# Optimization experiments

Hardware: AMD Instinct MI355X
Metric: run time of the kernel (lower is better)

The kernel has to match this reference:

```python
import jax, jax.numpy as jnp
import numpy as np

EPS = 1e-9
LAM_SEL, LAM_ID, LAM_RATE, LAM_KL, LAM_ENT, LAM_SMOOTH = 1.0, 10.0, 5.0, 0.1, 0.05, 0.5


def setup_inputs() -> dict:
    T, BS, V, K, RIDS = 48, 256, 4096, 32, 1024
    key = jax.random.key(0)
    ks = jax.random.split(key, 10)
    selector_logits = jax.random.normal(ks[0], (BS, 2, K), dtype=jnp.float32)
    selector_probs = jax.nn.softmax(jax.random.normal(ks[1], (BS, 2, K)), axis=-1)
    sel_idx = jax.random.randint(ks[2], (BS, 2), 0, K)
    selector_onehot = jax.nn.one_hot(sel_idx, K, dtype=jnp.float32)
    out_ids = jax.nn.softmax(jax.random.normal(ks[3], (T, BS, V)), axis=-1)
    out_rates = jax.random.uniform(ks[4], (T, BS, 1), dtype=jnp.float32)
    lab_idx = jax.random.randint(ks[5], (T + 2, BS), 0, V)
    trg_labels = jax.nn.one_hot(lab_idx, V, dtype=jnp.float32)
    trg_rates = jax.random.uniform(ks[6], (T + 2, BS, 1), dtype=jnp.float32)
    trg_lengths = jax.random.randint(ks[7], (BS,), 4, T + 2).astype(jnp.int32)
    candi_ids = jax.random.randint(ks[8], (BS, 2, K), 0, RIDS).astype(jnp.int32)
    routes = jax.random.randint(ks[9], (BS, V), 0, RIDS).astype(jnp.int32)
    return {
        'selector_logits': selector_logits, 'selector_probs': selector_probs,
        'selector_onehot': selector_onehot, 'out_ids': out_ids, 'out_rates': out_rates,
        'trg_labels': trg_labels, 'trg_rates': trg_rates, 'trg_lengths': trg_lengths,
        'candi_ids': candi_ids, 'routes': routes,
    }


def _align(lab, T_pred):
    T_lab = lab.shape[0]
    if T_lab >= T_pred + 2:
        return lab[1:-1]
    elif T_lab == T_pred:
        return lab
    else:
        pad = T_pred - T_lab
        return jnp.concatenate([lab, jnp.repeat(lab[-1:], pad, axis=0)], axis=0)


def _loss(selector_logits, selector_probs, selector_onehot, out_ids, out_rates,
          trg_labels, trg_rates, trg_lengths, candi_ids, routes):
    bs, _, K = selector_probs.shape
    # --- selector NLL (use_bce_logits=False path) ---
    sel_mask = (selector_onehot.sum(-1) > 0.5).astype(jnp.float32)      # [bs,2]
    sel_p_true = jnp.maximum((selector_probs * selector_onehot).sum(-1), EPS)
    loss_sel = (-jnp.log(sel_p_true) * sel_mask).sum() / jnp.maximum(sel_mask.sum(), 1.0)

    # --- id NLL over aligned target labels ---
    T_pred = out_ids.shape[0]
    tla = _align(trg_labels, T_pred)                                    # [T,bs,V]
    tra = _align(trg_rates, T_pred)                                     # [T,bs,1]
    step_mask = (tla.sum(-1) > 0.5).astype(jnp.float32)                 # [T,bs]
    p_true = jnp.maximum((out_ids * tla).sum(-1), EPS)
    loss_id = (-jnp.log(p_true) * step_mask).sum() * LAM_ID / jnp.maximum(step_mask.sum(), 1.0)

    # --- rate L1 ---
    denom_rate = jnp.maximum(1, (trg_lengths - 2).sum()).astype(jnp.float32)
    loss_rate = jnp.abs(out_rates - tra).sum() * LAM_RATE / denom_rate

    # --- KL over per-batch candidate unions (vectorized dedup via first-occurrence) ---
    U2 = 2 * K
    ids = candi_ids.reshape(bs, U2)                                     # [bs,2K]
    probs_flat = selector_probs.reshape(bs, U2)                         # [bs,2K]
    eq = ids[:, :, None] == ids[:, None, :]                             # [bs,2K,2K]
    rep = jnp.argmax(eq, axis=-1)                                       # first occurrence idx
    slots = jnp.arange(U2)
    valid = (rep == slots[None, :]).astype(jnp.float32)                 # [bs,2K] union slots
    Ucnt = valid.sum(-1)                                                # [bs]
    # Pm: scatter-add selector probs onto union slots (duplicates summed)
    rep_oh = (rep[:, :, None] == slots[None, None, :]).astype(jnp.float32)  # [bs,2K,2K]
    Pm = jnp.einsum('biu,bi->bu', rep_oh, probs_flat)                   # [bs,2K]
    Pm = Pm / jnp.maximum(Pm.sum(-1, keepdims=True), EPS)
    # Pb: project route mass onto union ids
    dist_r = out_ids.sum(0)                                             # [bs,V]
    match = (routes[:, :, None] == ids[:, None, :]).astype(jnp.float32)  # [bs,V,2K]
    agg = jnp.einsum('bvu,bv->bu', match, dist_r) * valid               # [bs,2K]
    s = agg.sum(-1, keepdims=True)                                      # [bs,1]
    uniform = valid / jnp.maximum(Ucnt, 1.0)[:, None]
    Pb = jnp.where(s > 0, agg / jnp.maximum(s, EPS), uniform)
    Pb_c = jnp.maximum(Pb, EPS)
    kl_b = (Pb_c * (jnp.log(Pb_c) - jnp.log(jnp.maximum(Pm, EPS))) * valid).sum(-1)
    loss_kl = LAM_KL * (kl_b.sum() / max(1, bs))

    # --- entropy of selector probs ---
    p = jnp.maximum(selector_probs, EPS)                                # [bs,2,K]
    ent_b = 0.5 * (-(p * jnp.log(p)).sum(-1)).sum(-1)                   # [bs]
    loss_entropy = LAM_ENT * (ent_b.sum() / max(1, bs))

    # --- rate smoothness ---
    r = out_rates[..., 0]                                               # [T,bs]
    dr = jnp.abs(r[1:] - r[:-1])                                        # [T-1,bs]
    eff = jnp.maximum(trg_lengths - 3, 0)                               # [bs]
    smask = (jnp.arange(T_pred - 1)[:, None] < eff[None, :]).astype(jnp.float32)
    loss_smooth = LAM_SMOOTH * (dr * smask).sum()

    return LAM_SEL * loss_sel + loss_id + loss_rate + loss_kl + loss_entropy + loss_smooth


def reference(selector_logits, selector_probs, selector_onehot, out_ids, out_rates,
              trg_labels, trg_rates, trg_lengths, candi_ids, routes):
    return _loss(selector_logits, selector_probs, selector_onehot, out_ids, out_rates,
                 trg_labels, trg_rates, trg_lengths, candi_ids, routes)
```

## Files before the change

kernel.cpp:

```cpp
#include <hip/hip_runtime.h>
#include <math.h>

#define EPSF 1e-9f

typedef float v4f __attribute__((ext_vector_type(4)));


__global__ __launch_bounds__(256) void e2e3_prep(
    const float* __restrict__ selector_probs,
    const int*   __restrict__ candi_ids,
    const int*   __restrict__ routes,
    float* __restrict__ pmlog_g,
    float* __restrict__ valid_g,
    signed char* __restrict__ slot_map)
{
    const int b   = blockIdx.x;
    const int tid = threadIdx.x;

    __shared__ int   ids_s[64];
    __shared__ int   table[1024];
    __shared__ int   rep_s[64];

    for (int i = tid; i < 1024; i += 256) table[i] = 64;
    if (tid < 64) ids_s[tid] = candi_ids[b * 64 + tid];
    __syncthreads();
    if (tid < 64) atomicMin(&table[ids_s[tid]], tid);
    __syncthreads();
    if (tid < 64) {
        const int r = table[ids_s[tid]];
        rep_s[tid] = r;
        valid_g[b * 64 + tid] = (r == tid) ? 1.f : 0.f;
    }
    __syncthreads();
    if (tid < 64) {
        float pm = 0.f;
        for (int i = 0; i < 64; ++i)
            if (rep_s[i] == tid) pm += selector_probs[b * 64 + i];
        float tot = pm;
        #pragma unroll
        for (int off = 32; off >= 1; off >>= 1) tot += __shfl_xor(tot, off, 64);
        pm = pm / fmaxf(tot, EPSF);
        pmlog_g[b * 64 + tid] = logf(fmaxf(pm, EPSF));
    }

    const int4* rp = reinterpret_cast<const int4*>(routes + (size_t)b * 4096 + tid * 16);
    signed char smv[16];
    #pragma unroll
    for (int j = 0; j < 4; ++j) {
        const int4 rv = rp[j];
        const int t0 = table[rv.x], t1 = table[rv.y], t2 = table[rv.z], t3 = table[rv.w];
        smv[j * 4 + 0] = (signed char)(t0 < 64 ? t0 : -1);
        smv[j * 4 + 1] = (signed char)(t1 < 64 ? t1 : -1);
        smv[j * 4 + 2] = (signed char)(t2 < 64 ? t2 : -1);
        smv[j * 4 + 3] = (signed char)(t3 < 64 ? t3 : -1);
    }
    *reinterpret_cast<int4*>(slot_map + (size_t)b * 4096 + tid * 16) =
        *reinterpret_cast<const int4*>(smv);
}

__global__ __launch_bounds__(512) void e2e3_stream(
    const float* __restrict__ out_ids,
    const float* __restrict__ trg_labels,
    const signed char* __restrict__ slot_map,
    float* __restrict__ agg_g,
    float* __restrict__ acc)
{
    const int bid  = blockIdx.x;
    const int b    = bid & 255;
    const int g    = bid >> 8;
    const int tid  = threadIdx.x;
    const int wave = tid >> 6;
    const int lane = tid & 63;
    const int v0   = tid << 3;
    const int t0   = g * 12;

    __shared__ float agg_s[64];
    __shared__ float red[2][8];
    if (tid < 64) agg_s[tid] = 0.f;
    __syncthreads();

    const size_t tstride = (size_t)256 * 4096;
    const float* outp = out_ids    + (size_t)t0 * tstride       + (size_t)b * 4096 + v0;
    const float* labp = trg_labels + (size_t)(t0 + 1) * tstride + (size_t)b * 4096 + v0;

    v4f d0 = (v4f)(0.f);
    v4f d1 = (v4f)(0.f);
    float idnum = 0.f, idcnt = 0.f;

    v4f o0 = *reinterpret_cast<const v4f*>(outp);
    v4f o1 = *reinterpret_cast<const v4f*>(outp + 4);
    v4f l0 = __builtin_nontemporal_load(reinterpret_cast<const v4f*>(labp));
    v4f l1 = __builtin_nontemporal_load(reinterpret_cast<const v4f*>(labp + 4));

    for (int t = 0; t < 12; ++t) {
        v4f no0 = o0, no1 = o1, nl0 = l0, nl1 = l1;
        if (t < 11) {
            const size_t off = (size_t)(t + 1) * tstride;
            no0 = *reinterpret_cast<const v4f*>(outp + off);
            no1 = *reinterpret_cast<const v4f*>(outp + off + 4);
            nl0 = __builtin_nontemporal_load(reinterpret_cast<const v4f*>(labp + off));
            nl1 = __builtin_nontemporal_load(reinterpret_cast<const v4f*>(labp + off + 4));
        }
        d0 += o0;
        d1 += o1;
        if (l0.x > 0.5f) { idnum -= logf(fmaxf(o0.x, EPSF)); idcnt += 1.f; }
        if (l0.y > 0.5f) { idnum -= logf(fmaxf(o0.y, EPSF)); idcnt += 1.f; }
        if (l0.z > 0.5f) { idnum -= logf(fmaxf(o0.z, EPSF)); idcnt += 1.f; }
        if (l0.w > 0.5f) { idnum -= logf(fmaxf(o0.w, EPSF)); idcnt += 1.f; }
        if (l1.x > 0.5f) { idnum -= logf(fmaxf(o1.x, EPSF)); idcnt += 1.f; }
        if (l1.y > 0.5f) { idnum -= logf(fmaxf(o1.y, EPSF)); idcnt += 1.f; }
        if (l1.z > 0.5f) { idnum -= logf(fmaxf(o1.z, EPSF)); idcnt += 1.f; }
        if (l1.w > 0.5f) { idnum -= logf(fmaxf(o1.w, EPSF)); idcnt += 1.f; }
        o0 = no0; o1 = no1; l0 = nl0; l1 = nl1;
    }

    {
        const uint2 sv = *reinterpret_cast<const uint2*>(slot_map + (size_t)b * 4096 + v0);
        const unsigned int w0 = sv.x, w1 = sv.y;
        const float dv[8] = {d0.x, d0.y, d0.z, d0.w, d1.x, d1.y, d1.z, d1.w};
        #pragma unroll
        for (int j = 0; j < 4; ++j) {
            const int u0 = (int)(signed char)((w0 >> (8 * j)) & 0xFF);
            if (u0 >= 0) atomicAdd(&agg_s[u0], dv[j]);
            const int u1 = (int)(signed char)((w1 >> (8 * j)) & 0xFF);
            if (u1 >= 0) atomicAdd(&agg_s[u1], dv[4 + j]);
        }
    }

    #pragma unroll
    for (int off = 32; off >= 1; off >>= 1) {
        idnum += __shfl_down(idnum, off, 64);
        idcnt += __shfl_down(idcnt, off, 64);
    }
    if (lane == 0) { red[0][wave] = idnum; red[1][wave] = idcnt; }
    __syncthreads();
    if (tid == 0) {
        float a = 0.f, c = 0.f;
        #pragma unroll
        for (int w = 0; w < 8; ++w) { a += red[0][w]; c += red[1][w]; }
        atomicAdd(&acc[0], a);
        atomicAdd(&acc[1], c);
    }
    if (tid < 64) atomicAdd(&agg_g[b * 64 + tid], agg_s[tid]);
}

__global__ __launch_bounds__(64) void e2e3_kl2(
    const float* __restrict__ agg_g,
    const float* __restrict__ pmlog_g,
    const float* __restrict__ valid_g,
    float* __restrict__ acc)
{
    const int b = blockIdx.x;
    const int u = threadIdx.x;

    const float va = valid_g[b * 64 + u];
    const float a  = (va > 0.5f) ? agg_g[b * 64 + u] : 0.f;
    float s = a, uc = va;
    #pragma unroll
    for (int off = 32; off >= 1; off >>= 1) {
        s  += __shfl_xor(s,  off, 64);
        uc += __shfl_xor(uc, off, 64);
    }
    const float pb = (s > 0.f) ? (a / fmaxf(s, EPSF)) : (va / fmaxf(uc, 1.f));
    float term = 0.f;
    if (va > 0.5f) {
        const float pbc = fmaxf(pb, EPSF);
        term = pbc * (logf(pbc) - pmlog_g[b * 64 + u]);
    }
    #pragma unroll
    for (int off = 32; off >= 1; off >>= 1) term += __shfl_down(term, off, 64);
    if (u == 0) atomicAdd(&acc[2], term);
}

__global__ __launch_bounds__(256) void e2e3_small(
    const float* __restrict__ selector_probs,
    const float* __restrict__ selector_onehot,
    const float* __restrict__ out_rates,
    const float* __restrict__ trg_rates,
    const int*   __restrict__ trg_lengths,
    const float* __restrict__ acc,
    float* __restrict__ out)
{
    const int tid  = threadIdx.x;
    const int wave = tid >> 6;
    const int lane = tid & 63;

    float v_selnum = 0.f, v_selcnt = 0.f, v_ent = 0.f;
    float v_rate = 0.f, v_den = 0.f, v_smooth = 0.f;

    for (int g = tid; g < 512; g += 256) {
        const float* pp = selector_probs  + g * 32;
        const float* oo = selector_onehot + g * 32;
        float p = 0.f, m = 0.f;
        #pragma unroll
        for (int k = 0; k < 32; ++k) { p += pp[k] * oo[k]; m += oo[k]; }
        if (m > 0.5f) { v_selnum += -logf(fmaxf(p, EPSF)); v_selcnt += 1.f; }
    }
    for (int i = tid; i < 256 * 64; i += 256) {
        const float p = fmaxf(selector_probs[i], EPSF);
        v_ent += -p * logf(p);
    }
    for (int i = tid; i < 48 * 256; i += 256)
        v_rate += fabsf(out_rates[i] - trg_rates[i + 256]);
    for (int b2 = tid; b2 < 256; b2 += 256)
        v_den += (float)(trg_lengths[b2] - 2);
    for (int i = tid; i < 47 * 256; i += 256) {
        const int b2 = i & 255;
        const int t  = i >> 8;
        int eff = trg_lengths[b2] - 3; if (eff < 0) eff = 0;
        if (t < eff) v_smooth += fabsf(out_rates[i + 256] - out_rates[i]);
    }

    __shared__ float red[6][4];
    float vals[6] = {v_selnum, v_selcnt, v_ent, v_rate, v_den, v_smooth};
    #pragma unroll
    for (int k = 0; k < 6; ++k) {
        float v = vals[k];
        #pragma unroll
        for (int off = 32; off >= 1; off >>= 1) v += __shfl_down(v, off, 64);
        if (lane == 0) red[k][wave] = v;
    }
    __syncthreads();
    if (tid == 0) {
        float s[6];
        #pragma unroll
        for (int k = 0; k < 6; ++k) s[k] = red[k][0] + red[k][1] + red[k][2] + red[k][3];
        const float loss =
              s[0] / fmaxf(s[1], 1.f)
            + 10.f * acc[0] / fmaxf(acc[1], 1.f)
            + 5.f  * s[3]   / fmaxf(s[4], 1.f)
            + 0.1f * acc[2] * (1.f / 256.f)
            + 0.05f * 0.5f * s[2] * (1.f / 256.f)
            + 0.5f * s[5];
        out[0] = loss;
    }
}

extern "C" void kernel_launch(void* const* d_in, const int* in_sizes, int n_in,
                              void* d_out, int out_size, void* d_ws, size_t ws_size,
                              hipStream_t stream) {
    const float* selector_probs  = (const float*)d_in[1];
    const float* selector_onehot = (const float*)d_in[2];
    const float* out_ids         = (const float*)d_in[3];
    const float* out_rates       = (const float*)d_in[4];
    const float* trg_labels      = (const float*)d_in[5];
    const float* trg_rates       = (const float*)d_in[6];
    const int*   trg_lengths     = (const int*)d_in[7];
    const int*   candi_ids       = (const int*)d_in[8];
    const int*   routes          = (const int*)d_in[9];

    char* ws = (char*)d_ws;
    float*       acc      = (float*)ws;
    float*       agg_g    = (float*)(ws + 256);
    float*       pmlog_g  = (float*)(ws + 256 + 65536);
    float*       valid_g  = (float*)(ws + 256 + 131072);
    signed char* slot_map = (signed char*)(ws + 256 + 196608);

    (void)hipMemsetAsync(ws, 0, 256 + 65536, stream);

    e2e3_prep<<<256, 256, 0, stream>>>(selector_probs, candi_ids, routes,
                                       pmlog_g, valid_g, slot_map);
    e2e3_stream<<<1024, 512, 0, stream>>>(out_ids, trg_labels, slot_map,
                                          agg_g, acc);
    e2e3_kl2<<<256, 64, 0, stream>>>(agg_g, pmlog_g, valid_g, acc);
    e2e3_small<<<1, 256, 0, stream>>>(selector_probs, selector_onehot,
                                      out_rates, trg_rates, trg_lengths,
                                      acc, (float*)d_out);
}
```

Baseline: 122.1 us.

## Split label scan into hot-index kernel and gather id NLL in streaming pass

A new kernel scans each one-hot label row once and records the index of its hot entry. The out_ids streaming kernel then no longer reads labels; it does one gather and one log per timestep for the NLL instead of a compare and possible log for every element. It also now prefetches two timesteps ahead. Total label and out_ids traffic stays the same but is split across two launches. The scan assumes at most one hot entry per row, and the extra launch adds a dependency.

```diff
diff --git a/kernel.cpp b/kernel.cpp
--- a/kernel.cpp
+++ b/kernel.cpp
@@ -58,10 +58,42 @@
         *reinterpret_cast<const int4*>(smv);
 }
 
-__global__ __launch_bounds__(512) void e2e3_stream(
+__global__ __launch_bounds__(256) void e2e3_hot(
+    const float* __restrict__ trg_labels,
+    int* __restrict__ hot_idx)
+{
+    const int wave = threadIdx.x >> 6;
+    const int lane = threadIdx.x & 63;
+    const int row  = blockIdx.x * 4 + wave;
+    const int t    = row >> 8;
+    const int b    = row & 255;
+
+    const size_t tstride = (size_t)256 * 4096;
+    const float* p = trg_labels + (size_t)(t + 1) * tstride + (size_t)b * 4096;
+
+    int hp = -1;
+    #pragma unroll
+    for (int j = 0; j < 16; ++j) {
+        const int base = j * 256 + lane * 4;
+        const v4f v = __builtin_nontemporal_load(
+            reinterpret_cast<const v4f*>(p + base));
+        if (v.x > 0.5f) hp = base;
+        if (v.y > 0.5f) hp = base + 1;
+        if (v.z > 0.5f) hp = base + 2;
+        if (v.w > 0.5f) hp = base + 3;
+    }
+    #pragma unroll
+    for (int off = 32; off >= 1; off >>= 1) {
+        const int o = __shfl_xor(hp, off, 64);
+        hp = (o > hp) ? o : hp;
+    }
+    if (lane == 0) hot_idx[row] = hp;
+}
+
+__global__ __launch_bounds__(512) void e2e3_dist(
     const float* __restrict__ out_ids,
-    const float* __restrict__ trg_labels,
     const signed char* __restrict__ slot_map,
+    const int*   __restrict__ hot_idx,
     float* __restrict__ agg_g,
     float* __restrict__ acc)
 {
@@ -69,49 +101,40 @@
     const int b    = bid & 255;
     const int g    = bid >> 8;
     const int tid  = threadIdx.x;
-    const int wave = tid >> 6;
-    const int lane = tid & 63;
     const int v0   = tid << 3;
     const int t0   = g * 12;
 
     __shared__ float agg_s[64];
-    __shared__ float red[2][8];
     if (tid < 64) agg_s[tid] = 0.f;
     __syncthreads();
 
     const size_t tstride = (size_t)256 * 4096;
-    const float* outp = out_ids    + (size_t)t0 * tstride       + (size_t)b * 4096 + v0;
-    const float* labp = trg_labels + (size_t)(t0 + 1) * tstride + (size_t)b * 4096 + v0;
-
-    v4f d0 = (v4f)(0.f);
-    v4f d1 = (v4f)(0.f);
-    float idnum = 0.f, idcnt = 0.f;
-
-    v4f o0 = *reinterpret_cast<const v4f*>(outp);
-    v4f o1 = *reinterpret_cast<const v4f*>(outp + 4);
-    v4f l0 = __builtin_nontemporal_load(reinterpret_cast<const v4f*>(labp));
-    v4f l1 = __builtin_nontemporal_load(reinterpret_cast<const v4f*>(labp + 4));
-
-    for (int t = 0; t < 12; ++t) {
-        v4f no0 = o0, no1 = o1, nl0 = l0, nl1 = l1;
-        if (t < 11) {
-            const size_t off = (size_t)(t + 1) * tstride;
-            no0 = *reinterpret_cast<const v4f*>(outp + off);
-            no1 = *reinterpret_cast<const v4f*>(outp + off + 4);
-            nl0 = __builtin_nontemporal_load(reinterpret_cast<const v4f*>(labp + off));
-            nl1 = __builtin_nontemporal_load(reinterpret_cast<const v4f*>(labp + off + 4));
-        }
-        d0 += o0;
-        d1 += o1;
-        if (l0.x > 0.5f) { idnum -= logf(fmaxf(o0.x, EPSF)); idcnt += 1.f; }
-        if (l0.y > 0.5f) { idnum -= logf(fmaxf(o0.y, EPSF)); idcnt += 1.f; }
-        if (l0.z > 0.5f) { idnum -= logf(fmaxf(o0.z, EPSF)); idcnt += 1.f; }
-        if (l0.w > 0.5f) { idnum -= logf(fmaxf(o0.w, EPSF)); idcnt += 1.f; }
-        if (l1.x > 0.5f) { idnum -= logf(fmaxf(o1.x, EPSF)); idcnt += 1.f; }
-        if (l1.y > 0.5f) { idnum -= logf(fmaxf(o1.y, EPSF)); idcnt += 1.f; }
-        if (l1.z > 0.5f) { idnum -= logf(fmaxf(o1.z, EPSF)); idcnt += 1.f; }
-        if (l1.w > 0.5f) { idnum -= logf(fmaxf(o1.w, EPSF)); idcnt += 1.f; }
-        o0 = no0; o1 = no1; l0 = nl0; l1 = nl1;
+
+    float gval = -1.f;
+    if (tid < 12) {
+        const int hid = hot_idx[(t0 + tid) * 256 + b];
+        if (hid >= 0)
+            gval = out_ids[(size_t)(t0 + tid) * tstride + (size_t)b * 4096 + hid];
+    }
+
+    const float* outp = out_ids + (size_t)t0 * tstride + (size_t)b * 4096 + v0;
+
+    v4f d0 = (v4f)(0.f), d1 = (v4f)(0.f);
+    v4f a0 = *reinterpret_cast<const v4f*>(outp);
+    v4f a1 = *reinterpret_cast<const v4f*>(outp + 4);
+    v4f b0 = *reinterpret_cast<const v4f*>(outp + tstride);
+    v4f b1 = *reinterpret_cast<const v4f*>(outp + tstride + 4);
+
+    for (int tt = 0; tt < 12; ++tt) {
+        v4f n0 = (v4f)(0.f), n1 = (v4f)(0.f);
+        if (tt < 10) {
+            const size_t off = (size_t)(tt + 2) * tstride;
+            n0 = *reinterpret_cast<const v4f*>(outp + off);
+            n1 = *reinterpret_cast<const v4f*>(outp + off + 4);
+        }
+        d0 += a0;
+        d1 += a1;
+        a0 = b0; a1 = b1; b0 = n0; b1 = n1;
     }
 
     {
@@ -127,20 +150,21 @@
         }
     }
 
-    #pragma unroll
-    for (int off = 32; off >= 1; off >>= 1) {
-        idnum += __shfl_down(idnum, off, 64);
-        idcnt += __shfl_down(idcnt, off, 64);
-    }
-    if (lane == 0) { red[0][wave] = idnum; red[1][wave] = idcnt; }
-    __syncthreads();
-    if (tid == 0) {
-        float a = 0.f, c = 0.f;
-        #pragma unroll
-        for (int w = 0; w < 8; ++w) { a += red[0][w]; c += red[1][w]; }
-        atomicAdd(&acc[0], a);
-        atomicAdd(&acc[1], c);
-    }
+    float idnum = (gval >= 0.f) ? -logf(fmaxf(gval, EPSF)) : 0.f;
+    float idcnt = (gval >= 0.f) ? 1.f : 0.f;
+    if (tid < 64) {
+        #pragma unroll
+        for (int off = 32; off >= 1; off >>= 1) {
+            idnum += __shfl_down(idnum, off, 64);
+            idcnt += __shfl_down(idcnt, off, 64);
+        }
+        if (tid == 0 && (idnum != 0.f || idcnt != 0.f)) {
+            atomicAdd(&acc[0], idnum);
+            atomicAdd(&acc[1], idcnt);
+        }
+    }
+
+    __syncthreads();
     if (tid < 64) atomicAdd(&agg_g[b * 64 + tid], agg_s[tid]);
 }
 
@@ -254,14 +278,16 @@
     float*       agg_g    = (float*)(ws + 256);
     float*       pmlog_g  = (float*)(ws + 256 + 65536);
     float*       valid_g  = (float*)(ws + 256 + 131072);
-    signed char* slot_map = (signed char*)(ws + 256 + 196608);
+    signed char* slot_map = (signed char*)(ws + 196864);
+    int*         hot_idx  = (int*)(ws + 1245440);
 
     (void)hipMemsetAsync(ws, 0, 256 + 65536, stream);
 
     e2e3_prep<<<256, 256, 0, stream>>>(selector_probs, candi_ids, routes,
                                        pmlog_g, valid_g, slot_map);
-    e2e3_stream<<<1024, 512, 0, stream>>>(out_ids, trg_labels, slot_map,
-                                          agg_g, acc);
+    e2e3_hot<<<3072, 256, 0, stream>>>(trg_labels, hot_idx);
+    e2e3_dist<<<1024, 512, 0, stream>>>(out_ids, slot_map, hot_idx,
+                                        agg_g, acc);
     e2e3_kl2<<<256, 64, 0, stream>>>(agg_g, pmlog_g, valid_g, acc);
     e2e3_small<<<1, 256, 0, stream>>>(selector_probs, selector_onehot,
                                       out_rates, trg_rates, trg_lengths,
```

Measured after the change: 131.7 us. 7.9% more time.
